# Kernel optimization log

Hardware: AMD Instinct MI355X
Metric: run time of the kernel (lower is better)

## Reference

```python
import jax, jax.numpy as jnp
import numpy as np

EMB = 4096
HEADS = 32
SCALE = 4
D = EMB // HEADS          # qkv_dim = 128
HKV = HEADS // SCALE      # 8 kv heads
B, S = 2, 2048


def setup_inputs() -> dict:
    key = jax.random.key(0)
    ks = jax.random.split(key, 7)
    std = 0.02
    return {
        "x": jax.random.normal(ks[0], (B, S, EMB), jnp.float32),
        "Wq": jax.random.normal(ks[1], (EMB, D, HEADS), jnp.float32) * std,
        "bq": jnp.zeros((D, HEADS), jnp.float32),
        "Wk": jax.random.normal(ks[2], (EMB, D, HKV), jnp.float32) * std,
        "bk": jnp.zeros((D, HKV), jnp.float32),
        "Wv": jax.random.normal(ks[3], (EMB, D, HKV), jnp.float32) * std,
        "bv": jnp.zeros((D, HKV), jnp.float32),
    }


def reference(x, Wq, bq, Wk, bk, Wv, bv):
    # DenseGeneral projections: (B,S,E) -> (B,S,D,H)
    q = jnp.einsum("bse,edh->bsdh", x, Wq) + bq          # [B,S,D,H]
    k = jnp.einsum("bse,edh->bsdh", x, Wk) + bk          # [B,S,D,Hkv]
    v = jnp.einsum("bse,edh->bsdh", x, Wv) + bv          # [B,S,D,Hkv]
    # repeat kv heads (each kv head duplicated SCALE times, matching jnp.repeat)
    k = jnp.repeat(k, SCALE, axis=-1)                    # [B,S,D,H]
    v = jnp.repeat(v, SCALE, axis=-1)                    # [B,S,D,H]
    # NOTE: as written in the source, attention contracts the HEAD axis per
    # token: scores are (qkv_dim x qkv_dim) per (b, s) position.
    scores = jnp.einsum("bsdh,bseh->bsde", q, k) / np.float32(np.sqrt(D))
    attn = jax.nn.softmax(scores, axis=-1)               # [B,S,D,D]
    out = jnp.einsum("bsde,bseh->bsdh", attn, v)         # [B,S,D,H]
    return out.reshape(x.shape[:-1] + (EMB,))
```

## Files before the change

### kernel.cpp

```cpp
#include <hip/hip_runtime.h>
#include <cstdint>

typedef unsigned short ushort_t;
typedef __bf16 bf16x8 __attribute__((ext_vector_type(8)));
typedef float f32x4 __attribute__((ext_vector_type(4)));

__device__ __forceinline__ unsigned short f2bf(float f) {
  unsigned u = __builtin_bit_cast(unsigned, f);
  u += 0x7FFFu + ((u >> 16) & 1u);
  return (unsigned short)(u >> 16);
}
__device__ __forceinline__ float bflo(unsigned u) {
  return __builtin_bit_cast(float, u << 16);
}
__device__ __forceinline__ float bfhi(unsigned u) {
  return __builtin_bit_cast(float, u & 0xFFFF0000u);
}
__device__ __forceinline__ void gld16(const void* g, void* l) {
  auto* gp = reinterpret_cast<const __attribute__((address_space(1))) unsigned*>(
      reinterpret_cast<uintptr_t>(g));
  auto* lp = reinterpret_cast<__attribute__((address_space(3))) unsigned*>(
      reinterpret_cast<uintptr_t>(l));
  __builtin_amdgcn_global_load_lds(gp, lp, 16, 0, 0);
}

__global__ __launch_bounds__(256) void prep_all(
    const float* __restrict__ x, const float* __restrict__ Wq,
    const float* __restrict__ Wk, const float* __restrict__ Wv,
    const float* __restrict__ bq, const float* __restrict__ bk,
    const float* __restrict__ bv, ushort_t* __restrict__ Ax,
    ushort_t* __restrict__ Wt, float* __restrict__ bias) {
  __shared__ ushort_t red[64][65];
  const int b = blockIdx.x;
  const int tid = threadIdx.x;
  if (b < 3072) {
    const int ntile = b % 48, ktile = b / 48;
    const int n0 = ntile * 64, k0 = ktile * 64;
    if (ntile < 16) {
      for (int i = tid; i < 64 * 64; i += 256) {
        const int kk = i >> 6, nn = i & 63;
        const float4 w = *reinterpret_cast<const float4*>(
            Wq + (size_t)(k0 + kk) * 4096 + (size_t)(n0 + nn) * 4);
        red[kk][nn] = f2bf(w.x + w.y + w.z + w.w);
      }
    } else {
      const float* W = (ntile < 32) ? Wk : Wv;
      const int nb = (ntile < 32) ? (n0 - 1024) : (n0 - 2048);
      for (int i = tid; i < 64 * 64; i += 256) {
        const int kk = i >> 6, nn = i & 63;
        red[kk][nn] = f2bf(W[(size_t)(k0 + kk) * 1024 + nb + nn]);
      }
    }
    __syncthreads();
    for (int i = tid; i < 64 * 64; i += 256) {
      const int kk = i & 63, nn = i >> 6;
      Wt[(size_t)(n0 + nn) * 4096 + k0 + kk] = red[kk][nn];
    }
  } else if (b < 11264) {
    const size_t i = ((size_t)(b - 3072) * 256 + tid) * 8;
    const float4 a = *reinterpret_cast<const float4*>(x + i);
    const float4 c = *reinterpret_cast<const float4*>(x + i + 4);
    union { ushort_t u[8]; uint4 v; } pk;
    pk.u[0] = f2bf(a.x); pk.u[1] = f2bf(a.y); pk.u[2] = f2bf(a.z); pk.u[3] = f2bf(a.w);
    pk.u[4] = f2bf(c.x); pk.u[5] = f2bf(c.y); pk.u[6] = f2bf(c.z); pk.u[7] = f2bf(c.w);
    *reinterpret_cast<uint4*>(Ax + i) = pk.v;
  } else {
    const int n = (b - 11264) * 256 + tid;
    float v;
    if (n < 1024) {
      const float4 w = *reinterpret_cast<const float4*>(bq + (size_t)n * 4);
      v = w.x + w.y + w.z + w.w;
    } else if (n < 2048) {
      v = bk[n - 1024];
    } else {
      v = bv[n - 2048];
    }
    bias[n] = v;
  }
}

#define WAITV0() asm volatile("s_waitcnt vmcnt(0)" ::: "memory")
#define BARRIER()                         \
  do {                                    \
    __builtin_amdgcn_s_barrier();         \
    asm volatile("" ::: "memory");        \
    __builtin_amdgcn_sched_barrier(0);    \
  } while (0)

__global__ __launch_bounds__(512, 2) void gemm_qkv(const ushort_t* __restrict__ A,
                                                   const ushort_t* __restrict__ Bt,
                                                   const float* __restrict__ bias,
                                                   ushort_t* __restrict__ C) {
  __shared__ char smem[114688];
  ushort_t* AsBuf = reinterpret_cast<ushort_t*>(smem);
  ushort_t* BsBuf = reinterpret_cast<ushort_t*>(smem + 65536);
  const int tid = threadIdx.x;
  const int lane = tid & 63, wave = tid >> 6;

  const int id = blockIdx.x;
  const int wg = (id & 7) * 32 + (id >> 3);
  const int M0 = (wg >> 4) * 256, N0 = (wg & 15) * 192;

  const int rik = lane >> 3;
  const int gch = (lane & 7) ^ rik;
  const ushort_t* aG = A + (size_t)(M0 + wave * 32 + rik) * 4096 + gch * 8;
  const ushort_t* bG = Bt + (size_t)(N0 + wave * 24 + rik) * 4096 + gch * 8;

  const int kh = wave & 1, wq = wave >> 1;
  const int wm = wq >> 1, wn = wq & 1;
  const int quad = lane >> 4, l15 = lane & 15;

  const int ch = ((kh * 4 + quad) ^ (l15 & 7)) * 16;
  const int abase = (wm * 128 + l15) * 128 + ch;
  const int bbase = (wn * 96 + l15) * 128 + ch;

  f32x4 acc[8][6];
  const f32x4 z = {0.f, 0.f, 0.f, 0.f};
#pragma unroll
  for (int mi = 0; mi < 8; ++mi)
#pragma unroll
    for (int ni = 0; ni < 6; ++ni) acc[mi][ni] = z;

  auto stage = [&](int bb, int kt) {
    const int ko = kt * 64;
    ushort_t* asb = AsBuf + bb * 16384;
    ushort_t* bsb = BsBuf + bb * 12288;
#pragma unroll
    for (int q = 0; q < 4; ++q)
      gld16(aG + ko + (size_t)q * (8 * 4096), asb + (wave * 4 + q) * 512);
#pragma unroll
    for (int q = 0; q < 3; ++q)
      gld16(bG + ko + (size_t)q * (8 * 4096), bsb + (wave * 3 + q) * 512);
  };

  stage(0, 0);
  WAITV0();
  BARRIER();

  for (int kt = 0; kt < 64; ++kt) {
    const int bb = kt & 1;
    if (kt < 63) stage(bb ^ 1, kt + 1);
    const char* ab = reinterpret_cast<const char*>(AsBuf + bb * 16384);
    const char* bbp = reinterpret_cast<const char*>(BsBuf + bb * 12288);
    bf16x8 af[8];
#pragma unroll
    for (int mi = 0; mi < 8; ++mi)
      af[mi] = *reinterpret_cast<const bf16x8*>(ab + abase + mi * 2048);
#pragma unroll
    for (int ni = 0; ni < 6; ++ni) {
      const bf16x8 bf = *reinterpret_cast<const bf16x8*>(bbp + bbase + ni * 2048);
      __builtin_amdgcn_s_setprio(1);
#pragma unroll
      for (int mi = 0; mi < 8; ++mi)
        acc[mi][ni] =
            __builtin_amdgcn_mfma_f32_16x16x32_bf16(af[mi], bf, acc[mi][ni], 0, 0, 0);
      __builtin_amdgcn_s_setprio(0);
    }
    WAITV0();
    BARRIER();
  }

  float* scr = reinterpret_cast<float*>(smem);
  const int slot = (wq * 64 + lane) * 97;
#pragma unroll
  for (int p = 0; p < 2; ++p) {
    __syncthreads();
    if (kh == 1) {
#pragma unroll
      for (int mi = 0; mi < 4; ++mi)
#pragma unroll
        for (int ni = 0; ni < 6; ++ni)
#pragma unroll
          for (int r = 0; r < 4; ++r)
            scr[slot + (mi * 6 + ni) * 4 + r] = acc[p * 4 + mi][ni][r];
    }
    __syncthreads();
    if (kh == 0) {
#pragma unroll
      for (int ni = 0; ni < 6; ++ni) {
        const int cc = N0 + wn * 96 + ni * 16 + l15;
        const float bn = bias[cc];
#pragma unroll
        for (int mi = 0; mi < 4; ++mi) {
          const int gmi = p * 4 + mi;
          const int r0 = M0 + wm * 128 + gmi * 16 + quad * 4;
#pragma unroll
          for (int r = 0; r < 4; ++r)
            C[(size_t)(r0 + r) * 3072 + cc] =
                f2bf(acc[gmi][ni][r] + scr[slot + (mi * 6 + ni) * 4 + r] + bn);
        }
      }
    }
  }
}

__global__ __launch_bounds__(256, 4) void attn_tok(const ushort_t* __restrict__ C,
                                                   float* __restrict__ out) {
  __shared__ uint4 kv4[4][256];
  const int tid = threadIdx.x;
  const int lane = tid & 63, wv = tid >> 6;
  const int t = blockIdx.x * 4 + wv;
  const ushort_t* Crow = C + (size_t)t * 3072;

  const uint4* src = reinterpret_cast<const uint4*>(Crow + 1024);
#pragma unroll
  for (int r = 0; r < 4; ++r) kv4[wv][r * 64 + lane] = src[r * 64 + lane];
  __syncthreads();

  const uint4 q01 = *reinterpret_cast<const uint4*>(Crow + lane * 16);
  const uint4 q23 = *reinterpret_cast<const uint4*>(Crow + lane * 16 + 8);
  float qa[8], qb[8];
  qa[0] = bflo(q01.x); qa[1] = bfhi(q01.x); qa[2] = bflo(q01.y); qa[3] = bfhi(q01.y);
  qa[4] = bflo(q01.z); qa[5] = bfhi(q01.z); qa[6] = bflo(q01.w); qa[7] = bfhi(q01.w);
  qb[0] = bflo(q23.x); qb[1] = bfhi(q23.x); qb[2] = bflo(q23.y); qb[3] = bfhi(q23.y);
  qb[4] = bflo(q23.z); qb[5] = bfhi(q23.z); qb[6] = bflo(q23.w); qb[7] = bfhi(q23.w);

  const uint4* kvw = kv4[wv];
  const float sc = 0.08838834764831845f;
  float oa[8], ob[8];
#pragma unroll
  for (int j = 0; j < 8; ++j) { oa[j] = 0.f; ob[j] = 0.f; }
  float l0 = 0.f, l1 = 0.f;

#pragma unroll 2
  for (int e = 0; e < 128; ++e) {
    const uint4 kr = kvw[e];
    float kf[8];
    kf[0] = bflo(kr.x); kf[1] = bfhi(kr.x); kf[2] = bflo(kr.y); kf[3] = bfhi(kr.y);
    kf[4] = bflo(kr.z); kf[5] = bfhi(kr.z); kf[6] = bflo(kr.w); kf[7] = bfhi(kr.w);
    float s0 = 0.f, s1 = 0.f;
#pragma unroll
    for (int j = 0; j < 8; ++j) { s0 += qa[j] * kf[j]; s1 += qb[j] * kf[j]; }
    const float p0 = __expf(s0 * sc);
    const float p1 = __expf(s1 * sc);
    l0 += p0; l1 += p1;
    const uint4 vr = kvw[128 + e];
    float vf[8];
    vf[0] = bflo(vr.x); vf[1] = bfhi(vr.x); vf[2] = bflo(vr.y); vf[3] = bfhi(vr.y);
    vf[4] = bflo(vr.z); vf[5] = bfhi(vr.z); vf[6] = bflo(vr.w); vf[7] = bfhi(vr.w);
#pragma unroll
    for (int j = 0; j < 8; ++j) { oa[j] += p0 * vf[j]; ob[j] += p1 * vf[j]; }
  }

  const float i0 = 1.f / l0, i1 = 1.f / l1;
  float4* dst = reinterpret_cast<float4*>(out + (size_t)t * 4096 + (size_t)lane * 64);
#pragma unroll
  for (int j = 0; j < 8; ++j) {
    const float w = oa[j] * i0;
    dst[j] = make_float4(w, w, w, w);
  }
#pragma unroll
  for (int j = 0; j < 8; ++j) {
    const float w = ob[j] * i1;
    dst[8 + j] = make_float4(w, w, w, w);
  }
}

extern "C" void kernel_launch(void* const* d_in, const int* in_sizes, int n_in,
                              void* d_out, int out_size, void* d_ws, size_t ws_size,
                              hipStream_t stream) {
  const float* x  = (const float*)d_in[0];
  const float* Wq = (const float*)d_in[1];
  const float* bq = (const float*)d_in[2];
  const float* Wk = (const float*)d_in[3];
  const float* bk = (const float*)d_in[4];
  const float* Wv = (const float*)d_in[5];
  const float* bv = (const float*)d_in[6];
  float* out = (float*)d_out;

  ushort_t* Ax = (ushort_t*)d_out;
  ushort_t* Wt = Ax + (size_t)4096 * 4096;
  float* bias = (float*)(Wt + (size_t)3072 * 4096);
  ushort_t* Cmat = (ushort_t*)d_ws;

  prep_all<<<dim3(11276), 256, 0, stream>>>(x, Wq, Wk, Wv, bq, bk, bv, Ax, Wt, bias);
  gemm_qkv<<<dim3(256), 512, 0, stream>>>(Ax, Wt, bias, Cmat);
  attn_tok<<<dim3(1024), 256, 0, stream>>>(Cmat, out);
}
```

Before: 351.6 us.

## Software-pipeline LDS fragment loads one k-step ahead of MFMA compute

Restructures the GEMM main loop so that the register fragments for k-tile t+1 are read from LDS while the MFMAs for tile t run, with global-to-LDS staging issued two tiles ahead into the buffer just consumed. Fragments are double-buffered in registers (two Frags structs), and the loop is unrolled by two to swap them. This aims to hide LDS read latency behind matrix-core work. In exchange it roughly doubles the fragment register footprint, which under launch_bounds(512,2) with a 48-tile accumulator risks spills or lower occupancy.

```diff
diff --git a/kernel.cpp b/kernel.cpp
--- a/kernel.cpp
+++ b/kernel.cpp
@@ -80,12 +80,18 @@
 }
 
 #define WAITV0() asm volatile("s_waitcnt vmcnt(0)" ::: "memory")
+#define DRAIN() asm volatile("s_waitcnt vmcnt(0) lgkmcnt(0)" ::: "memory")
 #define BARRIER()                         \
   do {                                    \
     __builtin_amdgcn_s_barrier();         \
     asm volatile("" ::: "memory");        \
     __builtin_amdgcn_sched_barrier(0);    \
   } while (0)
+
+struct Frags {
+  bf16x8 a[8];
+  bf16x8 b[6];
+};
 
 __global__ __launch_bounds__(512, 2) void gemm_qkv(const ushort_t* __restrict__ A,
                                                    const ushort_t* __restrict__ Bt,
@@ -132,33 +138,49 @@
     for (int q = 0; q < 3; ++q)
       gld16(bG + ko + (size_t)q * (8 * 4096), bsb + (wave * 3 + q) * 512);
   };
-
+  auto ldFrags = [&](Frags& F, int bb) {
+    const char* ab = reinterpret_cast<const char*>(AsBuf + bb * 16384);
+    const char* bbp = reinterpret_cast<const char*>(BsBuf + bb * 12288);
+#pragma unroll
+    for (int mi = 0; mi < 8; ++mi)
+      F.a[mi] = *reinterpret_cast<const bf16x8*>(ab + abase + mi * 2048);
+#pragma unroll
+    for (int ni = 0; ni < 6; ++ni)
+      F.b[ni] = *reinterpret_cast<const bf16x8*>(bbp + bbase + ni * 2048);
+  };
+  auto mmqAll = [&](const Frags& F) {
+#pragma unroll
+    for (int ni = 0; ni < 6; ++ni) {
+      __builtin_amdgcn_s_setprio(1);
+#pragma unroll
+      for (int mi = 0; mi < 8; ++mi)
+        acc[mi][ni] =
+            __builtin_amdgcn_mfma_f32_16x16x32_bf16(F.a[mi], F.b[ni], acc[mi][ni], 0, 0, 0);
+      __builtin_amdgcn_s_setprio(0);
+    }
+  };
+  auto body = [&](int t, Frags& Fc, Frags& Fn) {
+    DRAIN();
+    BARRIER();
+    if (t + 2 <= 63) stage(t & 1, t + 2);
+    ldFrags(Fn, (t + 1) & 1);
+    mmqAll(Fc);
+  };
+
+  Frags F0, F1;
   stage(0, 0);
   WAITV0();
   BARRIER();
-
-  for (int kt = 0; kt < 64; ++kt) {
-    const int bb = kt & 1;
-    if (kt < 63) stage(bb ^ 1, kt + 1);
-    const char* ab = reinterpret_cast<const char*>(AsBuf + bb * 16384);
-    const char* bbp = reinterpret_cast<const char*>(BsBuf + bb * 12288);
-    bf16x8 af[8];
-#pragma unroll
-    for (int mi = 0; mi < 8; ++mi)
-      af[mi] = *reinterpret_cast<const bf16x8*>(ab + abase + mi * 2048);
-#pragma unroll
-    for (int ni = 0; ni < 6; ++ni) {
-      const bf16x8 bf = *reinterpret_cast<const bf16x8*>(bbp + bbase + ni * 2048);
-      __builtin_amdgcn_s_setprio(1);
-#pragma unroll
-      for (int mi = 0; mi < 8; ++mi)
-        acc[mi][ni] =
-            __builtin_amdgcn_mfma_f32_16x16x32_bf16(af[mi], bf, acc[mi][ni], 0, 0, 0);
-      __builtin_amdgcn_s_setprio(0);
-    }
-    WAITV0();
-    BARRIER();
-  }
+  ldFrags(F0, 0);
+  stage(1, 1);
+
+  for (int t = 0; t < 62; t += 2) {
+    body(t, F0, F1);
+    body(t + 1, F1, F0);
+  }
+  body(62, F0, F1);
+  DRAIN();
+  mmqAll(F1);
 
   float* scr = reinterpret_cast<float*>(smem);
   const int slot = (wq * 64 + lane) * 97;
```

Measured after the change: 1.082 ms. +207.7%, slower.
